# Kernel optimization log

Hardware: AMD Instinct MI355X
Metric: run time of the kernel (lower is better)

The kernel has to match this reference:

```python
import jax, jax.numpy as jnp
import numpy as np

N_NODES = 50000
N_EDGES = 800000
IN_DIM = 128
HID = 128
N_GRAPHS = 64


def setup_inputs() -> dict:
    key = jax.random.key(0)
    ks = jax.random.split(key, 12)
    edge_index = jax.random.randint(ks[0], (2, N_EDGES), 0, N_NODES, dtype=jnp.int64)
    edge_weight = jax.random.uniform(ks[1], (N_EDGES,), dtype=jnp.float32)
    input_feature = jax.random.normal(ks[2], (N_NODES, IN_DIM), dtype=jnp.float32)
    graph_indicator = jnp.sort(jax.random.randint(ks[3], (N_NODES,), 0, N_GRAPHS, dtype=jnp.int64))
    s = 0.05
    W1 = jax.random.normal(ks[4], (IN_DIM, HID), dtype=jnp.float32) * s
    b1 = jnp.zeros((HID,), jnp.float32)
    W2 = jax.random.normal(ks[5], (HID, HID), dtype=jnp.float32) * s
    b2 = jnp.zeros((HID,), jnp.float32)
    W3 = jax.random.normal(ks[6], (HID, HID), dtype=jnp.float32) * s
    b3 = jnp.zeros((HID,), jnp.float32)
    wa = jax.random.normal(ks[7], (3 * HID, 1), dtype=jnp.float32) * s
    ba = jnp.zeros((1,), jnp.float32)
    Wf = jax.random.normal(ks[8], (3 * HID * 2, IN_DIM), dtype=jnp.float32) * s
    bf = jnp.zeros((IN_DIM,), jnp.float32)
    return dict(edge_index=edge_index, edge_weight=edge_weight,
                input_feature=input_feature, graph_indicator=graph_indicator,
                W1=W1, b1=b1, W2=W2, b2=b2, W3=W3, b3=b3,
                wa=wa, ba=ba, Wf=Wf, bf=bf)


def reference(edge_index, edge_weight, input_feature, graph_indicator,
              W1, b1, W2, b2, W3, b3, wa, ba, Wf, bf):
    src, dst = edge_index[0], edge_index[1]

    def gcn(x, W, b):
        # GraphConvolution: adj @ (x @ W) + b, adj given as weighted edge list
        support = x @ W  # [N, d_out]
        msg = edge_weight[:, None] * support[src]  # [E, d_out] gather
        return jax.ops.segment_sum(msg, dst, num_segments=N_NODES) + b

    g1 = jax.nn.relu(gcn(input_feature, W1, b1))
    g2 = jax.nn.relu(gcn(g1, W2, b2))
    g3 = jax.nn.relu(gcn(g2, W3, b3))
    h = jnp.concatenate([g1, g2, g3], axis=1)  # [N, 3*HID]

    # SelfAttentionPooling: attention score via a 1-dim GraphConvolution, tanh gate
    score = jnp.tanh(gcn(h, wa, ba))  # [N, 1]
    pool = h * score

    # segment avg / max pooling per graph
    seg_sum = jax.ops.segment_sum(pool, graph_indicator, num_segments=N_GRAPHS)
    counts = jax.ops.segment_sum(jnp.ones((N_NODES, 1), pool.dtype), graph_indicator,
                                 num_segments=N_GRAPHS)
    avg = seg_sum / jnp.maximum(counts, 1.0)
    mx = jax.ops.segment_max(pool, graph_indicator, num_segments=N_GRAPHS)
    pooled = jnp.concatenate([avg, mx], axis=1)  # [G, 6*HID]

    return jax.nn.relu(pooled @ Wf + bf)  # [G, IN_DIM]
```

## Files before the change

### kernel.cpp

```cpp
#include <hip/hip_runtime.h>
#include <math.h>

#define HID 128
#define POOL_SEG 16
#define WT_STRIDE 136
#define ELL_D 48
#define SC_CHUNK 2048
#define FXS 16384.0f
#define FXI (1.0f/16384.0f)

typedef __attribute__((ext_vector_type(8))) short short8;
typedef __attribute__((ext_vector_type(4))) float float4v;

__device__ inline short f2bf(float f) {
  unsigned u = __builtin_bit_cast(unsigned, f);
  unsigned r = (u + 0x7fff + ((u >> 16) & 1)) >> 16;
  return (short)r;
}
__device__ inline unsigned pack2bf(float lo, float hi) {
  return (unsigned)(unsigned short)f2bf(lo) | ((unsigned)(unsigned short)f2bf(hi) << 16);
}
__device__ inline float bflo(unsigned u) { return __builtin_bit_cast(float, u << 16); }
__device__ inline float bfhi(unsigned u) { return __builtin_bit_cast(float, u & 0xffff0000u); }
__device__ inline float bf2f(unsigned short s) { return __builtin_bit_cast(float, (unsigned)s << 16); }
__device__ inline unsigned short f2h(float f) {
  _Float16 h = (_Float16)f;
  return __builtin_bit_cast(unsigned short, h);
}
__device__ inline float h2f(unsigned short hb) {
  return (float)__builtin_bit_cast(_Float16, hb);
}

__global__ __launch_bounds__(256) void prologue(
    const void* __restrict__ ei_raw, const float* __restrict__ ew,
    int2* __restrict__ packed,
    const float* __restrict__ W1, const float* __restrict__ W2, const float* __restrict__ W3,
    short* __restrict__ T1, short* __restrict__ T2, short* __restrict__ T3,
    const void* __restrict__ gi_raw, int* __restrict__ gstart,
    int E, int N, int G, int EB) {
  int b = blockIdx.x, t = threadIdx.x;
  if (b < EB) {
    int e = b * 256 + t;
    if (e < E) {
      const int* pw = (const int*)ei_raw;
      int nz = 0;
#pragma unroll
      for (int i = 1; i < 64; i += 2) nz |= pw[i];
      int s, d;
      if (nz == 0) {
        const long long* p = (const long long*)ei_raw;
        s = (int)p[e]; d = (int)p[E + e];
      } else {
        const int* p = (const int*)ei_raw;
        s = p[e]; d = p[E + e];
      }
      packed[e] = make_int2((d << 16) | s, __builtin_bit_cast(int, ew[e]));
    }
  } else if (b < EB + 192) {
    int i = (b - EB) * 256 + t;
    int which = i >> 14, idx = i & 16383;
    int k = idx >> 7, nn = idx & 127;
    const float* W = (which == 0) ? W1 : ((which == 1) ? W2 : W3);
    short* T = (which == 0) ? T1 : ((which == 1) ? T2 : T3);
    T[nn * WT_STRIDE + k] = f2bf(W[idx]);
  } else {
    int g = t;
    if (g > G) return;
    if (g == G) { gstart[g] = N; return; }
    bool is64 = (((const int*)gi_raw)[N - 1] == 0);
    const long long* g64 = (const long long*)gi_raw;
    const int* g32 = (const int*)gi_raw;
    int lo = 0, hi = N;
    while (lo < hi) {
      int mid = (lo + hi) >> 1;
      long long v = is64 ? g64[mid] : (long long)g32[mid];
      if (v < (long long)g) lo = mid + 1; else hi = mid;
    }
    gstart[g] = lo;
  }
}

__global__ void scatter_ell(const int2* __restrict__ packed, int* __restrict__ cursor,
                            unsigned* __restrict__ ell, int E, int N) {
  int group = blockIdx.x & 7;
  int chunk = blockIdx.x >> 3;
  int rng = (N + 7) >> 3;
  int lo = group * rng;
  int hi = lo + rng; if (hi > N) hi = N;
  int base = chunk * SC_CHUNK;
  for (int i = 0; i < SC_CHUNK; i += 256) {
    int e = base + i + threadIdx.x;
    if (e < E) {
      int2 rec = packed[e];
      int d = ((unsigned)rec.x) >> 16;
      if (d >= lo && d < hi) {
        unsigned s = (unsigned)rec.x & 0xFFFFu;
        unsigned short wh = f2h(__builtin_bit_cast(float, rec.y));
        int pos = atomicAdd(&cursor[d], 1);
        if (pos < ELL_D)
          ell[(size_t)d * ELL_D + pos] = (s << 16) | (unsigned)wh;
      }
    }
  }
}

__global__ __launch_bounds__(256) void gemm_mfma(const float* __restrict__ Af,
                                                 const unsigned short* __restrict__ Abf,
                                                 const short* __restrict__ Wt,
                                                 unsigned short* __restrict__ C,
                                                 int n, int a_is_bf16) {
  __shared__ short Wlds[128 * WT_STRIDE];
  int t = threadIdx.x;
  {
    const ulonglong2* gsrc = (const ulonglong2*)Wt;
    ulonglong2* ldst = (ulonglong2*)Wlds;
    for (int i = t; i < (128 * WT_STRIDE) / 8; i += 256) ldst[i] = gsrc[i];
  }
  __syncthreads();

  int wave = t >> 6, lane = t & 63;
  int quad = lane >> 4, l15 = lane & 15;
  int m0 = blockIdx.x * 64 + wave * 16;
  size_t SL8 = (size_t)n * 16;

  int m = m0 + l15; if (m >= n) m = n - 1;
  short8 afrag[4];
  if (a_is_bf16) {
#pragma unroll
    for (int c = 0; c < 4; c++) {
      int k0 = c * 32 + quad * 8;
      afrag[c] = *(const short8*)(Abf + (size_t)(k0 >> 4) * SL8 + (size_t)m * 16 + (k0 & 15));
    }
  } else {
    const float* Arow = Af + (size_t)m * 128;
#pragma unroll
    for (int c = 0; c < 4; c++) {
      int k0 = c * 32 + quad * 8;
      float4 x = *(const float4*)(Arow + k0);
      float4 y = *(const float4*)(Arow + k0 + 4);
      short8 a;
      a[0] = f2bf(x.x); a[1] = f2bf(x.y); a[2] = f2bf(x.z); a[3] = f2bf(x.w);
      a[4] = f2bf(y.x); a[5] = f2bf(y.y); a[6] = f2bf(y.z); a[7] = f2bf(y.w);
      afrag[c] = a;
    }
  }

  float4v acc[8];
#pragma unroll
  for (int tt = 0; tt < 8; tt++) acc[tt] = (float4v){0.f, 0.f, 0.f, 0.f};

#pragma unroll
  for (int c = 0; c < 4; c++) {
    int kb = c * 32 + quad * 8;
#pragma unroll
    for (int tt = 0; tt < 8; tt++) {
      const short8* bp = (const short8*)&Wlds[(tt * 16 + l15) * WT_STRIDE + kb];
      acc[tt] = __builtin_amdgcn_mfma_f32_16x16x32_bf16(afrag[c], *bp, acc[tt], 0, 0, 0);
    }
  }

  int rbase = m0 + quad * 4;
#pragma unroll
  for (int tt = 0; tt < 8; tt++) {
    size_t sb = (size_t)tt * SL8;
#pragma unroll
    for (int r = 0; r < 4; r++) {
      int row = rbase + r;
      if (row < n) C[sb + (size_t)row * 16 + l15] = (unsigned short)f2bf(acc[tt][r]);
    }
  }
}

__global__ __launch_bounds__(256) void aggregate_sl(
    const unsigned short* __restrict__ support, const int* __restrict__ deg_arr,
    const unsigned* __restrict__ ell, const float* __restrict__ bias,
    unsigned short* __restrict__ out,
    const unsigned short* __restrict__ g1p, const unsigned short* __restrict__ g2p,
    const float* __restrict__ wa, int* __restrict__ s_pre_fx,
    int n, int do_score) {
  int slice = blockIdx.x & 7;
  int t = threadIdx.x;
  int node = (blockIdx.x >> 3) * 128 + (t >> 1);
  int q = t & 1;
  if (node >= n) return;

  int deg = deg_arr[node]; if (deg > ELL_D) deg = ELL_D;
  const unsigned* row = ell + (size_t)node * ELL_D;
  const uint4* sb = (const uint4*)support + (size_t)slice * n * 2 + q;

  float acc[8];
#pragma unroll
  for (int j = 0; j < 8; j++) acc[j] = 0.f;

  int i = 0;
  for (; i + 3 < deg; i += 4) {
    uint4 rr = *(const uint4*)(row + i);
    float w0 = h2f((unsigned short)(rr.x & 0xFFFF)) * FXS;
    float w1 = h2f((unsigned short)(rr.y & 0xFFFF)) * FXS;
    float w2 = h2f((unsigned short)(rr.z & 0xFFFF)) * FXS;
    float w3 = h2f((unsigned short)(rr.w & 0xFFFF)) * FXS;
    uint4 v0 = sb[(size_t)(rr.x >> 16) * 2];
    uint4 v1 = sb[(size_t)(rr.y >> 16) * 2];
    uint4 v2 = sb[(size_t)(rr.z >> 16) * 2];
    uint4 v3 = sb[(size_t)(rr.w >> 16) * 2];
    acc[0] += rintf(w0 * bflo(v0.x)); acc[1] += rintf(w0 * bfhi(v0.x));
    acc[2] += rintf(w0 * bflo(v0.y)); acc[3] += rintf(w0 * bfhi(v0.y));
    acc[4] += rintf(w0 * bflo(v0.z)); acc[5] += rintf(w0 * bfhi(v0.z));
    acc[6] += rintf(w0 * bflo(v0.w)); acc[7] += rintf(w0 * bfhi(v0.w));
    acc[0] += rintf(w1 * bflo(v1.x)); acc[1] += rintf(w1 * bfhi(v1.x));
    acc[2] += rintf(w1 * bflo(v1.y)); acc[3] += rintf(w1 * bfhi(v1.y));
    acc[4] += rintf(w1 * bflo(v1.z)); acc[5] += rintf(w1 * bfhi(v1.z));
    acc[6] += rintf(w1 * bflo(v1.w)); acc[7] += rintf(w1 * bfhi(v1.w));
    acc[0] += rintf(w2 * bflo(v2.x)); acc[1] += rintf(w2 * bfhi(v2.x));
    acc[2] += rintf(w2 * bflo(v2.y)); acc[3] += rintf(w2 * bfhi(v2.y));
    acc[4] += rintf(w2 * bflo(v2.z)); acc[5] += rintf(w2 * bfhi(v2.z));
    acc[6] += rintf(w2 * bflo(v2.w)); acc[7] += rintf(w2 * bfhi(v2.w));
    acc[0] += rintf(w3 * bflo(v3.x)); acc[1] += rintf(w3 * bfhi(v3.x));
    acc[2] += rintf(w3 * bflo(v3.y)); acc[3] += rintf(w3 * bfhi(v3.y));
    acc[4] += rintf(w3 * bflo(v3.z)); acc[5] += rintf(w3 * bfhi(v3.z));
    acc[6] += rintf(w3 * bflo(v3.w)); acc[7] += rintf(w3 * bfhi(v3.w));
  }
  for (; i < deg; i++) {
    unsigned r0 = row[i];
    float w0 = h2f((unsigned short)(r0 & 0xFFFF)) * FXS;
    uint4 v0 = sb[(size_t)(r0 >> 16) * 2];
    acc[0] += rintf(w0 * bflo(v0.x)); acc[1] += rintf(w0 * bfhi(v0.x));
    acc[2] += rintf(w0 * bflo(v0.y)); acc[3] += rintf(w0 * bfhi(v0.y));
    acc[4] += rintf(w0 * bflo(v0.z)); acc[5] += rintf(w0 * bfhi(v0.z));
    acc[6] += rintf(w0 * bflo(v0.w)); acc[7] += rintf(w0 * bfhi(v0.w));
  }

  float f[8];
#pragma unroll
  for (int j = 0; j < 8; j++) f[j] = acc[j] * FXI;

  float4 b0 = ((const float4*)bias)[slice * 4 + q * 2];
  float4 b1 = ((const float4*)bias)[slice * 4 + q * 2 + 1];
  f[0] = fmaxf(f[0] + b0.x, 0.f); f[1] = fmaxf(f[1] + b0.y, 0.f);
  f[2] = fmaxf(f[2] + b0.z, 0.f); f[3] = fmaxf(f[3] + b0.w, 0.f);
  f[4] = fmaxf(f[4] + b1.x, 0.f); f[5] = fmaxf(f[5] + b1.y, 0.f);
  f[6] = fmaxf(f[6] + b1.z, 0.f); f[7] = fmaxf(f[7] + b1.w, 0.f);

  uint4 o;
  o.x = pack2bf(f[0], f[1]); o.y = pack2bf(f[2], f[3]);
  o.z = pack2bf(f[4], f[5]); o.w = pack2bf(f[6], f[7]);
  ((uint4*)out)[(size_t)slice * n * 2 + (size_t)node * 2 + q] = o;

  if (do_score) {
    uint4 u1 = ((const uint4*)g1p)[(size_t)slice * n * 2 + (size_t)node * 2 + q];
    uint4 u2 = ((const uint4*)g2p)[(size_t)slice * n * 2 + (size_t)node * 2 + q];
    const float* wa1 = wa + slice * 16 + q * 8;
    const float* wa2 = wa1 + 128;
    const float* wa3 = wa1 + 256;
    float sc = bflo(u1.x) * wa1[0] + bfhi(u1.x) * wa1[1]
             + bflo(u1.y) * wa1[2] + bfhi(u1.y) * wa1[3]
             + bflo(u1.z) * wa1[4] + bfhi(u1.z) * wa1[5]
             + bflo(u1.w) * wa1[6] + bfhi(u1.w) * wa1[7]
             + bflo(u2.x) * wa2[0] + bfhi(u2.x) * wa2[1]
             + bflo(u2.y) * wa2[2] + bfhi(u2.y) * wa2[3]
             + bflo(u2.z) * wa2[4] + bfhi(u2.z) * wa2[5]
             + bflo(u2.w) * wa2[6] + bfhi(u2.w) * wa2[7];
#pragma unroll
    for (int j = 0; j < 8; j++) sc += f[j] * wa3[j];
    sc += __shfl_xor(sc, 1, 64);
    if (q == 0) atomicAdd(&s_pre_fx[node], __float2int_rn(sc * FXS));
  }
}

__global__ __launch_bounds__(384) void pool_partial(const unsigned short* __restrict__ g1,
                                                    const unsigned short* __restrict__ g2,
                                                    const unsigned short* __restrict__ g3,
                                                    const int* __restrict__ s_pre_fx,
                                                    const int* __restrict__ deg_arr,
                                                    const unsigned* __restrict__ ell,
                                                    const float* __restrict__ ba,
                                                    const int* __restrict__ gstart,
                                                    float* __restrict__ part, int n) {
  int g = blockIdx.x / POOL_SEG, seg = blockIdx.x % POOL_SEG;
  int t = threadIdx.x;
  int sg = t >> 7, dd = t & 127;
  const unsigned short* gp = (sg == 0) ? g1 : ((sg == 1) ? g2 : g3);
  const unsigned short* col = gp + (size_t)(dd >> 4) * ((size_t)n * 16) + (dd & 15);
  int s = gstart[g], e = gstart[g + 1];
  int len = e - s;
  int chunk = (len + POOL_SEG - 1) / POOL_SEG;
  int ns = s + seg * chunk;
  int ne = ns + chunk; if (ne > e) ne = e;
  float ba0 = ba[0];
  __shared__ float sc_lds[256];
  float sum = 0.f, mx = -3.402823466e38f;
  for (int tb = ns; tb < ne; tb += 256) {
    int te = tb + 256; if (te > ne) te = ne;
    __syncthreads();
    if (t < te - tb) {
      int node = tb + t;
      int deg = deg_arr[node]; if (deg > ELL_D) deg = ELL_D;
      const unsigned* row = ell + (size_t)node * ELL_D;
      float acc = 0.f;
      for (int i = 0; i < deg; i++) {
        unsigned r = row[i];
        acc += rintf(h2f((unsigned short)(r & 0xFFFF)) * (float)s_pre_fx[r >> 16]);
      }
      sc_lds[t] = tanhf(acc * FXI + ba0);
    }
    __syncthreads();
    for (int node = tb; node < te; node++) {
      float v = bf2f(col[(size_t)node * 16]) * sc_lds[node - tb];
      sum += v;
      mx = fmaxf(mx, v);
    }
  }
  size_t base = (size_t)blockIdx.x * 768;
  part[base + t] = sum;
  part[base + 384 + t] = mx;
}

__global__ __launch_bounds__(512) void tail(const float* __restrict__ part,
                                            const int* __restrict__ gstart,
                                            const float* __restrict__ Wf,
                                            const float* __restrict__ bfb,
                                            float* __restrict__ out) {
  __shared__ float pooled[768];
  __shared__ float red[512];
  int g = blockIdx.x, t = threadIdx.x;
  float cnt = (float)(gstart[g + 1] - gstart[g]);
  float inv = 1.0f / fmaxf(cnt, 1.0f);
  if (t < 384) {
    int d = t;
    float sum = 0.f, mx = -3.402823466e38f;
    for (int seg = 0; seg < POOL_SEG; seg++) {
      size_t base = ((size_t)g * POOL_SEG + seg) * 768;
      sum += part[base + d];
      mx = fmaxf(mx, part[base + 384 + d]);
    }
    pooled[d] = sum * inv;
    pooled[384 + d] = mx;
  }
  __syncthreads();
  int kc = t >> 7, c = t & 127;
  float acc = (kc == 0) ? bfb[c] : 0.f;
  int k0 = kc * 192;
#pragma unroll 8
  for (int k = k0; k < k0 + 192; k++) acc += pooled[k] * Wf[(size_t)k * 128 + c];
  red[t] = acc;
  __syncthreads();
  if (t < 128)
    out[(size_t)g * 128 + t] =
        fmaxf(red[t] + red[t + 128] + red[t + 256] + red[t + 384], 0.f);
}

extern "C" void kernel_launch(void* const* d_in, const int* in_sizes, int n_in,
                              void* d_out, int out_size, void* d_ws, size_t ws_size,
                              hipStream_t stream) {
  const void* ei_raw = d_in[0];
  const float* ew    = (const float*)d_in[1];
  const float* X     = (const float*)d_in[2];
  const void* gi_raw = d_in[3];
  const float* W1 = (const float*)d_in[4];  const float* b1 = (const float*)d_in[5];
  const float* W2 = (const float*)d_in[6];  const float* b2 = (const float*)d_in[7];
  const float* W3 = (const float*)d_in[8];  const float* b3 = (const float*)d_in[9];
  const float* wa = (const float*)d_in[10]; const float* ba = (const float*)d_in[11];
  const float* Wf = (const float*)d_in[12]; const float* bf = (const float*)d_in[13];
  float* out = (float*)d_out;

  const int E = in_sizes[1];
  const int N = in_sizes[2] / 128;
  const int G = out_size / 128;

  char* ws = (char*)d_ws;
  size_t off = 0;
  auto take = [&](size_t bytes) {
    char* p = ws + off;
    off = (off + bytes + 255) & ~(size_t)255;
    return p;
  };
  int* zb = (int*)take((size_t)N * 8);
  int* cursor   = zb;
  int* s_pre_fx = zb + N;
  int2* packed  = (int2*)take((size_t)E * 8);
  unsigned* ell = (unsigned*)take((size_t)N * ELL_D * 4);
  short*    wt1 = (short*)take((size_t)128 * WT_STRIDE * 2);
  short*    wt2 = (short*)take((size_t)128 * WT_STRIDE * 2);
  short*    wt3 = (short*)take((size_t)128 * WT_STRIDE * 2);
  unsigned short* support = (unsigned short*)take((size_t)N * 128 * 2);
  unsigned short* g1      = (unsigned short*)take((size_t)N * 128 * 2);
  unsigned short* g2      = (unsigned short*)take((size_t)N * 128 * 2);
  unsigned short* g3      = (unsigned short*)take((size_t)N * 128 * 2);
  int*   gstart  = (int*)take((size_t)(G + 1) * 4);
  float* part    = (float*)take((size_t)G * POOL_SEG * 768 * 4);
  if (off > ws_size) return;

  hipMemsetAsync(zb, 0, (size_t)N * 8, stream);

  const int EB = (E + 255) / 256;
  prologue<<<EB + 192 + 1, 256, 0, stream>>>(ei_raw, ew, packed,
                                             W1, W2, W3, wt1, wt2, wt3,
                                             gi_raw, gstart, E, N, G, EB);
  {
    int chunks = (E + SC_CHUNK - 1) / SC_CHUNK;
    scatter_ell<<<8 * chunks, 256, 0, stream>>>(packed, cursor, ell, E, N);
  }

  const int GB = (N + 63) / 64;
  const int AGB = 8 * ((N + 127) / 128);
  gemm_mfma<<<GB, 256, 0, stream>>>(X, (const unsigned short*)nullptr, wt1, support, N, 0);
  aggregate_sl<<<AGB, 256, 0, stream>>>(support, cursor, ell, b1, g1,
                                        nullptr, nullptr, nullptr, nullptr, N, 0);
  gemm_mfma<<<GB, 256, 0, stream>>>((const float*)nullptr, g1, wt2, support, N, 1);
  aggregate_sl<<<AGB, 256, 0, stream>>>(support, cursor, ell, b2, g2,
                                        nullptr, nullptr, nullptr, nullptr, N, 0);
  gemm_mfma<<<GB, 256, 0, stream>>>((const float*)nullptr, g2, wt3, support, N, 1);
  aggregate_sl<<<AGB, 256, 0, stream>>>(support, cursor, ell, b3, g3,
                                        g1, g2, wa, s_pre_fx, N, 1);

  pool_partial<<<G * POOL_SEG, 384, 0, stream>>>(g1, g2, g3, s_pre_fx, cursor, ell,
                                                 ba, gstart, part, N);
  tail<<<G, 512, 0, stream>>>(part, gstart, Wf, bf, out);
}
```

Measured before the change: 371.5 us.

## Switch feature layout to 32-column slices and split aggregation across node halves

Changes the sliced bf16 feature layout from 8 slices of 16 columns to 4 slices of 32 columns, so each gathered neighbor row is 64 contiguous bytes read by four lanes instead of 32 bytes read by two. The GEMM store/load indexing and pool_partial column indexing are updated to match. The aggregation grid is reorganized so each slice is processed by two block groups covering separate halves of the node range, and the score reduction gains an extra shuffle. Non-temporal loads and stores are added for ELL rows, degrees and outputs to reduce cache pollution. The aim is fewer, wider gather transactions per edge, at the cost of a larger working set per slice in cache.

```diff
diff --git a/kernel.cpp b/kernel.cpp
--- a/kernel.cpp
+++ b/kernel.cpp
@@ -11,6 +11,7 @@
 
 typedef __attribute__((ext_vector_type(8))) short short8;
 typedef __attribute__((ext_vector_type(4))) float float4v;
+typedef __attribute__((ext_vector_type(4))) unsigned uint4v;
 
 __device__ inline short f2bf(float f) {
   unsigned u = __builtin_bit_cast(unsigned, f);
@@ -121,16 +122,14 @@
   int wave = t >> 6, lane = t & 63;
   int quad = lane >> 4, l15 = lane & 15;
   int m0 = blockIdx.x * 64 + wave * 16;
-  size_t SL8 = (size_t)n * 16;
+  size_t SL = (size_t)n * 32;
 
   int m = m0 + l15; if (m >= n) m = n - 1;
   short8 afrag[4];
   if (a_is_bf16) {
 #pragma unroll
-    for (int c = 0; c < 4; c++) {
-      int k0 = c * 32 + quad * 8;
-      afrag[c] = *(const short8*)(Abf + (size_t)(k0 >> 4) * SL8 + (size_t)m * 16 + (k0 & 15));
-    }
+    for (int c = 0; c < 4; c++)
+      afrag[c] = *(const short8*)(Abf + c * SL + (size_t)m * 32 + quad * 8);
   } else {
     const float* Arow = Af + (size_t)m * 128;
 #pragma unroll
@@ -162,11 +161,12 @@
   int rbase = m0 + quad * 4;
 #pragma unroll
   for (int tt = 0; tt < 8; tt++) {
-    size_t sb = (size_t)tt * SL8;
+    int within = (tt & 1) * 16 + l15;
+    size_t sb = (size_t)(tt >> 1) * SL;
 #pragma unroll
     for (int r = 0; r < 4; r++) {
       int row = rbase + r;
-      if (row < n) C[sb + (size_t)row * 16 + l15] = (unsigned short)f2bf(acc[tt][r]);
+      if (row < n) C[sb + (size_t)row * 32 + within] = (unsigned short)f2bf(acc[tt][r]);
     }
   }
 }
@@ -177,16 +177,21 @@
     unsigned short* __restrict__ out,
     const unsigned short* __restrict__ g1p, const unsigned short* __restrict__ g2p,
     const float* __restrict__ wa, int* __restrict__ s_pre_fx,
-    int n, int do_score) {
-  int slice = blockIdx.x & 7;
+    int n, int halfN, int do_score) {
+  int group = blockIdx.x & 7;
+  int slice = group >> 1, half = group & 1;
+  int chunk = blockIdx.x >> 3;
   int t = threadIdx.x;
-  int node = (blockIdx.x >> 3) * 128 + (t >> 1);
-  int q = t & 1;
+  int local = chunk * 64 + (t >> 2);
+  int q = t & 3;
+  if (local >= halfN) return;
+  int node = half * halfN + local;
   if (node >= n) return;
 
-  int deg = deg_arr[node]; if (deg > ELL_D) deg = ELL_D;
+  int deg = __builtin_nontemporal_load(deg_arr + node);
+  if (deg > ELL_D) deg = ELL_D;
   const unsigned* row = ell + (size_t)node * ELL_D;
-  const uint4* sb = (const uint4*)support + (size_t)slice * n * 2 + q;
+  const uint4v* sb = (const uint4v*)support + (size_t)slice * n * 4 + q;
 
   float acc[8];
 #pragma unroll
@@ -194,75 +199,78 @@
 
   int i = 0;
   for (; i + 3 < deg; i += 4) {
-    uint4 rr = *(const uint4*)(row + i);
-    float w0 = h2f((unsigned short)(rr.x & 0xFFFF)) * FXS;
-    float w1 = h2f((unsigned short)(rr.y & 0xFFFF)) * FXS;
-    float w2 = h2f((unsigned short)(rr.z & 0xFFFF)) * FXS;
-    float w3 = h2f((unsigned short)(rr.w & 0xFFFF)) * FXS;
-    uint4 v0 = sb[(size_t)(rr.x >> 16) * 2];
-    uint4 v1 = sb[(size_t)(rr.y >> 16) * 2];
-    uint4 v2 = sb[(size_t)(rr.z >> 16) * 2];
-    uint4 v3 = sb[(size_t)(rr.w >> 16) * 2];
-    acc[0] += rintf(w0 * bflo(v0.x)); acc[1] += rintf(w0 * bfhi(v0.x));
-    acc[2] += rintf(w0 * bflo(v0.y)); acc[3] += rintf(w0 * bfhi(v0.y));
-    acc[4] += rintf(w0 * bflo(v0.z)); acc[5] += rintf(w0 * bfhi(v0.z));
-    acc[6] += rintf(w0 * bflo(v0.w)); acc[7] += rintf(w0 * bfhi(v0.w));
-    acc[0] += rintf(w1 * bflo(v1.x)); acc[1] += rintf(w1 * bfhi(v1.x));
-    acc[2] += rintf(w1 * bflo(v1.y)); acc[3] += rintf(w1 * bfhi(v1.y));
-    acc[4] += rintf(w1 * bflo(v1.z)); acc[5] += rintf(w1 * bfhi(v1.z));
-    acc[6] += rintf(w1 * bflo(v1.w)); acc[7] += rintf(w1 * bfhi(v1.w));
-    acc[0] += rintf(w2 * bflo(v2.x)); acc[1] += rintf(w2 * bfhi(v2.x));
-    acc[2] += rintf(w2 * bflo(v2.y)); acc[3] += rintf(w2 * bfhi(v2.y));
-    acc[4] += rintf(w2 * bflo(v2.z)); acc[5] += rintf(w2 * bfhi(v2.z));
-    acc[6] += rintf(w2 * bflo(v2.w)); acc[7] += rintf(w2 * bfhi(v2.w));
-    acc[0] += rintf(w3 * bflo(v3.x)); acc[1] += rintf(w3 * bfhi(v3.x));
-    acc[2] += rintf(w3 * bflo(v3.y)); acc[3] += rintf(w3 * bfhi(v3.y));
-    acc[4] += rintf(w3 * bflo(v3.z)); acc[5] += rintf(w3 * bfhi(v3.z));
-    acc[6] += rintf(w3 * bflo(v3.w)); acc[7] += rintf(w3 * bfhi(v3.w));
+    uint4v rr = __builtin_nontemporal_load((const uint4v*)(row + i));
+    float w0 = h2f((unsigned short)(rr[0] & 0xFFFF)) * FXS;
+    float w1 = h2f((unsigned short)(rr[1] & 0xFFFF)) * FXS;
+    float w2 = h2f((unsigned short)(rr[2] & 0xFFFF)) * FXS;
+    float w3 = h2f((unsigned short)(rr[3] & 0xFFFF)) * FXS;
+    uint4v v0 = sb[(size_t)(rr[0] >> 16) * 4];
+    uint4v v1 = sb[(size_t)(rr[1] >> 16) * 4];
+    uint4v v2 = sb[(size_t)(rr[2] >> 16) * 4];
+    uint4v v3 = sb[(size_t)(rr[3] >> 16) * 4];
+    acc[0] += rintf(w0 * bflo(v0[0])); acc[1] += rintf(w0 * bfhi(v0[0]));
+    acc[2] += rintf(w0 * bflo(v0[1])); acc[3] += rintf(w0 * bfhi(v0[1]));
+    acc[4] += rintf(w0 * bflo(v0[2])); acc[5] += rintf(w0 * bfhi(v0[2]));
+    acc[6] += rintf(w0 * bflo(v0[3])); acc[7] += rintf(w0 * bfhi(v0[3]));
+    acc[0] += rintf(w1 * bflo(v1[0])); acc[1] += rintf(w1 * bfhi(v1[0]));
+    acc[2] += rintf(w1 * bflo(v1[1])); acc[3] += rintf(w1 * bfhi(v1[1]));
+    acc[4] += rintf(w1 * bflo(v1[2])); acc[5] += rintf(w1 * bfhi(v1[2]));
+    acc[6] += rintf(w1 * bflo(v1[3])); acc[7] += rintf(w1 * bfhi(v1[3]));
+    acc[0] += rintf(w2 * bflo(v2[0])); acc[1] += rintf(w2 * bfhi(v2[0]));
+    acc[2] += rintf(w2 * bflo(v2[1])); acc[3] += rintf(w2 * bfhi(v2[1]));
+    acc[4] += rintf(w2 * bflo(v2[2])); acc[5] += rintf(w2 * bfhi(v2[2]));
+    acc[6] += rintf(w2 * bflo(v2[3])); acc[7] += rintf(w2 * bfhi(v2[3]));
+    acc[0] += rintf(w3 * bflo(v3[0])); acc[1] += rintf(w3 * bfhi(v3[0]));
+    acc[2] += rintf(w3 * bflo(v3[1])); acc[3] += rintf(w3 * bfhi(v3[1]));
+    acc[4] += rintf(w3 * bflo(v3[2])); acc[5] += rintf(w3 * bfhi(v3[2]));
+    acc[6] += rintf(w3 * bflo(v3[3])); acc[7] += rintf(w3 * bfhi(v3[3]));
   }
   for (; i < deg; i++) {
-    unsigned r0 = row[i];
+    unsigned r0 = __builtin_nontemporal_load(row + i);
     float w0 = h2f((unsigned short)(r0 & 0xFFFF)) * FXS;
-    uint4 v0 = sb[(size_t)(r0 >> 16) * 2];
-    acc[0] += rintf(w0 * bflo(v0.x)); acc[1] += rintf(w0 * bfhi(v0.x));
-    acc[2] += rintf(w0 * bflo(v0.y)); acc[3] += rintf(w0 * bfhi(v0.y));
-    acc[4] += rintf(w0 * bflo(v0.z)); acc[5] += rintf(w0 * bfhi(v0.z));
-    acc[6] += rintf(w0 * bflo(v0.w)); acc[7] += rintf(w0 * bfhi(v0.w));
+    uint4v v0 = sb[(size_t)(r0 >> 16) * 4];
+    acc[0] += rintf(w0 * bflo(v0[0])); acc[1] += rintf(w0 * bfhi(v0[0]));
+    acc[2] += rintf(w0 * bflo(v0[1])); acc[3] += rintf(w0 * bfhi(v0[1]));
+    acc[4] += rintf(w0 * bflo(v0[2])); acc[5] += rintf(w0 * bfhi(v0[2]));
+    acc[6] += rintf(w0 * bflo(v0[3])); acc[7] += rintf(w0 * bfhi(v0[3]));
   }
 
   float f[8];
 #pragma unroll
   for (int j = 0; j < 8; j++) f[j] = acc[j] * FXI;
 
-  float4 b0 = ((const float4*)bias)[slice * 4 + q * 2];
-  float4 b1 = ((const float4*)bias)[slice * 4 + q * 2 + 1];
+  float4 b0 = ((const float4*)bias)[slice * 8 + q * 2];
+  float4 b1 = ((const float4*)bias)[slice * 8 + q * 2 + 1];
   f[0] = fmaxf(f[0] + b0.x, 0.f); f[1] = fmaxf(f[1] + b0.y, 0.f);
   f[2] = fmaxf(f[2] + b0.z, 0.f); f[3] = fmaxf(f[3] + b0.w, 0.f);
   f[4] = fmaxf(f[4] + b1.x, 0.f); f[5] = fmaxf(f[5] + b1.y, 0.f);
   f[6] = fmaxf(f[6] + b1.z, 0.f); f[7] = fmaxf(f[7] + b1.w, 0.f);
 
-  uint4 o;
-  o.x = pack2bf(f[0], f[1]); o.y = pack2bf(f[2], f[3]);
-  o.z = pack2bf(f[4], f[5]); o.w = pack2bf(f[6], f[7]);
-  ((uint4*)out)[(size_t)slice * n * 2 + (size_t)node * 2 + q] = o;
+  uint4v o;
+  o[0] = pack2bf(f[0], f[1]); o[1] = pack2bf(f[2], f[3]);
+  o[2] = pack2bf(f[4], f[5]); o[3] = pack2bf(f[6], f[7]);
+  __builtin_nontemporal_store(o, (uint4v*)out + (size_t)slice * n * 4 + (size_t)node * 4 + q);
 
   if (do_score) {
-    uint4 u1 = ((const uint4*)g1p)[(size_t)slice * n * 2 + (size_t)node * 2 + q];
-    uint4 u2 = ((const uint4*)g2p)[(size_t)slice * n * 2 + (size_t)node * 2 + q];
-    const float* wa1 = wa + slice * 16 + q * 8;
+    uint4v u1 = __builtin_nontemporal_load(
+        (const uint4v*)g1p + (size_t)slice * n * 4 + (size_t)node * 4 + q);
+    uint4v u2 = __builtin_nontemporal_load(
+        (const uint4v*)g2p + (size_t)slice * n * 4 + (size_t)node * 4 + q);
+    const float* wa1 = wa + slice * 32 + q * 8;
     const float* wa2 = wa1 + 128;
     const float* wa3 = wa1 + 256;
-    float sc = bflo(u1.x) * wa1[0] + bfhi(u1.x) * wa1[1]
-             + bflo(u1.y) * wa1[2] + bfhi(u1.y) * wa1[3]
-             + bflo(u1.z) * wa1[4] + bfhi(u1.z) * wa1[5]
-             + bflo(u1.w) * wa1[6] + bfhi(u1.w) * wa1[7]
-             + bflo(u2.x) * wa2[0] + bfhi(u2.x) * wa2[1]
-             + bflo(u2.y) * wa2[2] + bfhi(u2.y) * wa2[3]
-             + bflo(u2.z) * wa2[4] + bfhi(u2.z) * wa2[5]
-             + bflo(u2.w) * wa2[6] + bfhi(u2.w) * wa2[7];
+    float sc = bflo(u1[0]) * wa1[0] + bfhi(u1[0]) * wa1[1]
+             + bflo(u1[1]) * wa1[2] + bfhi(u1[1]) * wa1[3]
+             + bflo(u1[2]) * wa1[4] + bfhi(u1[2]) * wa1[5]
+             + bflo(u1[3]) * wa1[6] + bfhi(u1[3]) * wa1[7]
+             + bflo(u2[0]) * wa2[0] + bfhi(u2[0]) * wa2[1]
+             + bflo(u2[1]) * wa2[2] + bfhi(u2[1]) * wa2[3]
+             + bflo(u2[2]) * wa2[4] + bfhi(u2[2]) * wa2[5]
+             + bflo(u2[3]) * wa2[6] + bfhi(u2[3]) * wa2[7];
 #pragma unroll
     for (int j = 0; j < 8; j++) sc += f[j] * wa3[j];
     sc += __shfl_xor(sc, 1, 64);
+    sc += __shfl_xor(sc, 2, 64);
     if (q == 0) atomicAdd(&s_pre_fx[node], __float2int_rn(sc * FXS));
   }
 }
@@ -280,7 +288,7 @@
   int t = threadIdx.x;
   int sg = t >> 7, dd = t & 127;
   const unsigned short* gp = (sg == 0) ? g1 : ((sg == 1) ? g2 : g3);
-  const unsigned short* col = gp + (size_t)(dd >> 4) * ((size_t)n * 16) + (dd & 15);
+  const unsigned short* col = gp + (size_t)(dd >> 5) * ((size_t)n * 32) + (dd & 31);
   int s = gstart[g], e = gstart[g + 1];
   int len = e - s;
   int chunk = (len + POOL_SEG - 1) / POOL_SEG;
@@ -305,7 +313,7 @@
     }
     __syncthreads();
     for (int node = tb; node < te; node++) {
-      float v = bf2f(col[(size_t)node * 16]) * sc_lds[node - tb];
+      float v = bf2f(col[(size_t)node * 32]) * sc_lds[node - tb];
       sum += v;
       mx = fmaxf(mx, v);
     }
@@ -402,16 +410,17 @@
   }
 
   const int GB = (N + 63) / 64;
-  const int AGB = 8 * ((N + 127) / 128);
+  const int halfN = (N + 1) / 2;
+  const int AGB = 8 * ((halfN + 63) / 64);
   gemm_mfma<<<GB, 256, 0, stream>>>(X, (const unsigned short*)nullptr, wt1, support, N, 0);
   aggregate_sl<<<AGB, 256, 0, stream>>>(support, cursor, ell, b1, g1,
-                                        nullptr, nullptr, nullptr, nullptr, N, 0);
+                                        nullptr, nullptr, nullptr, nullptr, N, halfN, 0);
   gemm_mfma<<<GB, 256, 0, stream>>>((const float*)nullptr, g1, wt2, support, N, 1);
   aggregate_sl<<<AGB, 256, 0, stream>>>(support, cursor, ell, b2, g2,
-                                        nullptr, nullptr, nullptr, nullptr, N, 0);
+                                        nullptr, nullptr, nullptr, nullptr, N, halfN, 0);
   gemm_mfma<<<GB, 256, 0, stream>>>((const float*)nullptr, g2, wt3, support, N, 1);
   aggregate_sl<<<AGB, 256, 0, stream>>>(support, cursor, ell, b3, g3,
-                                        g1, g2, wa, s_pre_fx, N, 1);
+                                        g1, g2, wa, s_pre_fx, N, halfN, 1);
 
   pool_partial<<<G * POOL_SEG, 384, 0, stream>>>(g1, g2, g3, s_pre_fx, cursor, ell,
                                                  ba, gstart, part, N);
```

Measured after the change: 374.8 us. No clear change (+0.9%).
